# Kernel tuning notes

Measured on AMD Instinct MI355X. Metric: run time of the kernel, lower is better.

Reference implementation:

```python
import jax, jax.numpy as jnp
import numpy as np

POOL = (7, 7)
CANONICAL_SIZE = 224.0


def _crop_and_resize(feat, boxes, box_idx, pool):
    # feat: [B,H,W,C], boxes: [R,4] normalized (y1,x1,y2,x2), box_idx: [R] int32
    # Matches tf.image.crop_and_resize(method='bilinear', extrapolation_value=0).
    H, W = feat.shape[1], feat.shape[2]
    ph, pw = pool
    y1, x1, y2, x2 = boxes[:, 0], boxes[:, 1], boxes[:, 2], boxes[:, 3]
    fy = jnp.arange(ph, dtype=feat.dtype) / (ph - 1)
    fx = jnp.arange(pw, dtype=feat.dtype) / (pw - 1)
    in_y = (y1[:, None] + fy[None, :] * (y2 - y1)[:, None]) * (H - 1)  # [R,ph]
    in_x = (x1[:, None] + fx[None, :] * (x2 - x1)[:, None]) * (W - 1)  # [R,pw]
    y0 = jnp.floor(in_y)
    x0 = jnp.floor(in_x)
    wy = (in_y - y0)[:, :, None, None]   # [R,ph,1,1]
    wx = (in_x - x0)[:, None, :, None]   # [R,1,pw,1]
    y0i = y0.astype(jnp.int32)
    x0i = x0.astype(jnp.int32)
    y0c = jnp.clip(y0i, 0, H - 1)
    y1c = jnp.clip(y0i + 1, 0, H - 1)
    x0c = jnp.clip(x0i, 0, W - 1)
    x1c = jnp.clip(x0i + 1, 0, W - 1)
    b = box_idx[:, None, None]

    def g(yc, xc):  # gather [R,ph,pw,C]
        return feat[b, yc[:, :, None], xc[:, None, :], :]

    top = g(y0c, x0c) * (1 - wx) + g(y0c, x1c) * wx
    bot = g(y1c, x0c) * (1 - wx) + g(y1c, x1c) * wx
    out = top * (1 - wy) + bot * wy
    valid = ((in_y >= 0) & (in_y <= H - 1))[:, :, None] & \
            ((in_x >= 0) & (in_x <= W - 1))[:, None, :]
    return out * valid[..., None].astype(feat.dtype)


def reference(rois, image_h, image_w, p2, p3, p4, p5):
    feats = (p2, p3, p4, p5)  # FPN levels 2..5
    B, N, _ = rois.shape
    R = B * N
    boxes = rois.reshape(R, 4)
    box_idx = jnp.repeat(jnp.arange(B, dtype=jnp.int32), N)
    h = boxes[:, 2] - boxes[:, 0]
    w = boxes[:, 3] - boxes[:, 1]
    img_area = jnp.asarray(image_h * image_w, dtype=jnp.float32)
    # Mask R-CNN FPN level assignment: 4 + log2(sqrt(h*w)/(224/sqrt(image_area)))
    spec = jnp.log2(jnp.sqrt(jnp.maximum(h * w, 1e-12)) /
                    (CANONICAL_SIZE / jnp.sqrt(img_area)))
    roi_level = jnp.clip(4 + jnp.round(spec).astype(jnp.int32), 2, 5)  # [R]
    boxes_sg = jax.lax.stop_gradient(boxes)
    # Pool every roi against every level, then select its assigned level.
    pooled_l = jnp.stack([_crop_and_resize(f, boxes_sg, box_idx, POOL)
                          for f in feats])  # [4,R,ph,pw,C]
    pooled = pooled_l[roi_level - 2, jnp.arange(R)]  # [R,ph,pw,C]
    # Original concatenates level-by-level (stable within-level flat order).
    perm = jnp.argsort(roi_level)  # jnp.argsort is stable
    return pooled[perm]


def setup_inputs() -> dict:
    key = jax.random.key(0)
    ks = jax.random.split(key, 8)
    B, N, C = 2, 1000, 256
    bh = jax.random.uniform(ks[0], (B, N), minval=0.02, maxval=0.5)
    bw = jax.random.uniform(ks[1], (B, N), minval=0.02, maxval=0.5)
    y1 = jax.random.uniform(ks[2], (B, N)) * (1.0 - bh)
    x1 = jax.random.uniform(ks[3], (B, N)) * (1.0 - bw)
    rois = jnp.stack([y1, x1, y1 + bh, x1 + bw], axis=-1).astype(jnp.float32)
    return {
        'rois': rois,
        'image_h': 1024,
        'image_w': 1024,
        'p2': jax.random.normal(ks[4], (B, 256, 256, C), dtype=jnp.float32),
        'p3': jax.random.normal(ks[5], (B, 128, 128, C), dtype=jnp.float32),
        'p4': jax.random.normal(ks[6], (B, 64, 64, C), dtype=jnp.float32),
        'p5': jax.random.normal(ks[7], (B, 32, 32, C), dtype=jnp.float32),
    }
```

## Files before the change

### kernel.cpp

```cpp
#include <hip/hip_runtime.h>
#include <math.h>


#define MAX_R 2048
#define NCHUNK_MAX (MAX_R / 64)

__global__ __launch_bounds__(1024)
void roi_setup_kernel(const float* __restrict__ rois,
                      const int* __restrict__ image_h,
                      const int* __restrict__ image_w,
                      int R,
                      int* __restrict__ level_out,
                      int* __restrict__ pos_out) {
    __shared__ int lvl_sh[MAX_R];
    __shared__ int wrank_sh[MAX_R];
    __shared__ int chunk_cnt[NCHUNK_MAX][4];
    __shared__ int chunk_base[NCHUNK_MAX][4];

    const int t    = threadIdx.x;
    const int lane = t & 63;
    const int wave = t >> 6;
    const int nwaves = blockDim.x >> 6;
    const int nchunk = (R + 63) / 64;

    const float canon = 224.0f / sqrtf((float)(image_h[0] * image_w[0]));

    for (int c = wave; c < nchunk; c += nwaves) {
        const int r = c * 64 + lane;
        int l = -1;
        if (r < R) {
            const float y1 = rois[r * 4 + 0];
            const float x1 = rois[r * 4 + 1];
            const float y2 = rois[r * 4 + 2];
            const float x2 = rois[r * 4 + 3];
            const float hw = (y2 - y1) * (x2 - x1);
            const float s = sqrtf(fmaxf(hw, 1e-12f));
            const double spec = log2((double)s / (double)canon);
            l = 4 + (int)rint(spec);
            l = min(5, max(2, l)) - 2;
            lvl_sh[r] = l;
        }
        unsigned long long m[4];
        #pragma unroll
        for (int i = 0; i < 4; ++i) m[i] = __ballot(l == i);
        if (r < R) {
            const unsigned long long below = (1ull << lane) - 1ull;
            wrank_sh[r] = __popcll(m[l] & below);
        }
        if (lane < 4) chunk_cnt[c][lane] = __popcll(m[lane]);
    }
    __syncthreads();

    if (t == 0) {
        int tot[4] = {0, 0, 0, 0};
        for (int c = 0; c < nchunk; ++c)
            for (int l = 0; l < 4; ++l) {
                chunk_base[c][l] = tot[l];
                tot[l] += chunk_cnt[c][l];
            }
        int base[4];
        int acc = 0;
        for (int l = 0; l < 4; ++l) { base[l] = acc; acc += tot[l]; }
        for (int c = 0; c < nchunk; ++c)
            for (int l = 0; l < 4; ++l) chunk_base[c][l] += base[l];
    }
    __syncthreads();

    for (int r = t; r < R; r += blockDim.x) {
        const int l = lvl_sh[r];
        level_out[r] = l;
        pos_out[r] = chunk_base[r >> 6][l] + wrank_sh[r];
    }
}

struct BinTask {
    const float4* f4;
    size_t i00, i01, i10, i11, oidx;
    float wx, wy, vmask;
};

__device__ __forceinline__ BinTask make_task(int work, int N,
        const float* __restrict__ rois,
        const int* __restrict__ level,
        const int* __restrict__ pos,
        const float* __restrict__ p2, const float* __restrict__ p3,
        const float* __restrict__ p4, const float* __restrict__ p5,
        int lane) {
    BinTask T;
    const int r   = work / 49;
    const int bin = work % 49;
    const int py  = bin / 7;
    const int px  = bin % 7;
    const int b   = r / N;

    const int l = level[r];
    const float* feat;
    int H;
    switch (l) {
        case 0:  feat = p2; H = 256; break;
        case 1:  feat = p3; H = 128; break;
        case 2:  feat = p4; H = 64;  break;
        default: feat = p5; H = 32;  break;
    }
    const int W = H;

    const float y1 = rois[r * 4 + 0];
    const float x1 = rois[r * 4 + 1];
    const float y2 = rois[r * 4 + 2];
    const float x2 = rois[r * 4 + 3];

    const float fy = (float)py / 6.0f;
    const float fx = (float)px / 6.0f;
    const float in_y = (y1 + fy * (y2 - y1)) * (float)(H - 1);
    const float in_x = (x1 + fx * (x2 - x1)) * (float)(W - 1);

    const float y0f = floorf(in_y);
    const float x0f = floorf(in_x);
    T.wy = in_y - y0f;
    T.wx = in_x - x0f;
    const int y0i = (int)y0f;
    const int x0i = (int)x0f;
    const int y0c = min(H - 1, max(0, y0i));
    const int y1c = min(H - 1, max(0, y0i + 1));
    const int x0c = min(W - 1, max(0, x0i));
    const int x1c = min(W - 1, max(0, x0i + 1));

    T.vmask = (in_y >= 0.0f && in_y <= (float)(H - 1) &&
               in_x >= 0.0f && in_x <= (float)(W - 1)) ? 1.0f : 0.0f;

    T.f4 = (const float4*)feat;
    const size_t bb = (size_t)b * H * W * 64;
    T.i00 = bb + ((size_t)y0c * W + x0c) * 64 + lane;
    T.i01 = bb + ((size_t)y0c * W + x1c) * 64 + lane;
    T.i10 = bb + ((size_t)y1c * W + x0c) * 64 + lane;
    T.i11 = bb + ((size_t)y1c * W + x1c) * 64 + lane;
    T.oidx = ((size_t)pos[r] * 49 + bin) * 64 + lane;
    return T;
}

__device__ __forceinline__ float4 blend(float4 v00, float4 v01,
                                        float4 v10, float4 v11,
                                        float wx, float wy, float vmask) {
    const float omwx = 1.0f - wx;
    const float omwy = 1.0f - wy;
    float4 res;
    res.x = ((v00.x * omwx + v01.x * wx) * omwy + (v10.x * omwx + v11.x * wx) * wy) * vmask;
    res.y = ((v00.y * omwx + v01.y * wx) * omwy + (v10.y * omwx + v11.y * wx) * wy) * vmask;
    res.z = ((v00.z * omwx + v01.z * wx) * omwy + (v10.z * omwx + v11.z * wx) * wy) * vmask;
    res.w = ((v00.w * omwx + v01.w * wx) * omwy + (v10.w * omwx + v11.w * wx) * wy) * vmask;
    return res;
}

__global__ __launch_bounds__(256)
void roi_align_kernel(const float* __restrict__ rois,
                      const float* __restrict__ p2,
                      const float* __restrict__ p3,
                      const float* __restrict__ p4,
                      const float* __restrict__ p5,
                      const int* __restrict__ level,
                      const int* __restrict__ pos,
                      float* __restrict__ out,
                      int N, int total) {
    const int lane   = threadIdx.x & 63;
    const int wave   = blockIdx.x * (blockDim.x >> 6) + (threadIdx.x >> 6);
    const int nwaves = gridDim.x * (blockDim.x >> 6);
    float4* __restrict__ o4 = (float4*)out;

    for (int w0 = wave * 2; w0 < total; w0 += nwaves * 2) {
        const bool hasB = (w0 + 1) < total;
        BinTask A = make_task(w0, N, rois, level, pos, p2, p3, p4, p5, lane);
        BinTask B = make_task(hasB ? w0 + 1 : w0, N, rois, level, pos, p2, p3, p4, p5, lane);

        const float4 a00 = A.f4[A.i00];
        const float4 a01 = A.f4[A.i01];
        const float4 a10 = A.f4[A.i10];
        const float4 a11 = A.f4[A.i11];
        const float4 b00 = B.f4[B.i00];
        const float4 b01 = B.f4[B.i01];
        const float4 b10 = B.f4[B.i10];
        const float4 b11 = B.f4[B.i11];

        o4[A.oidx] = blend(a00, a01, a10, a11, A.wx, A.wy, A.vmask);
        if (hasB)
            o4[B.oidx] = blend(b00, b01, b10, b11, B.wx, B.wy, B.vmask);
    }
}

extern "C" void kernel_launch(void* const* d_in, const int* in_sizes, int n_in,
                              void* d_out, int out_size, void* d_ws, size_t ws_size,
                              hipStream_t stream) {
    const float* rois = (const float*)d_in[0];
    const int*   ih   = (const int*)d_in[1];
    const int*   iw   = (const int*)d_in[2];
    const float* p2   = (const float*)d_in[3];
    const float* p3   = (const float*)d_in[4];
    const float* p4   = (const float*)d_in[5];
    const float* p5   = (const float*)d_in[6];

    const int R = in_sizes[0] / 4;
    const int B = in_sizes[3] / (256 * 256 * 256);
    const int N = R / B;
    const int total = R * 49;

    int* level = (int*)d_ws;
    int* pos   = level + R;

    roi_setup_kernel<<<1, 1024, 0, stream>>>(rois, ih, iw, R, level, pos);
    roi_align_kernel<<<2048, 256, 0, stream>>>(rois, p2, p3, p4, p5,
                                               level, pos, (float*)d_out, N, total);
}
```

Measured before the change: 264.5 us.

## Assign one ROI per block and use nontemporal output stores

The align kernel now launches one block per ROI instead of a grid-stride loop over flat bins. ROI-wide values (level, feature pointer, box coords, output base) are computed once per block, and each of the four waves handles bins b0 and b0+4 with a stride of 8. Output writes switch to nontemporal stores so the streaming output does not pollute the cache. This removes per-bin division and redundant level/pos/rois loads, but gives each block only 49 bins of work and a fixed R-sized grid.

```diff
diff --git a/kernel.cpp b/kernel.cpp
--- a/kernel.cpp
+++ b/kernel.cpp
@@ -4,6 +4,8 @@
 
 #define MAX_R 2048
 #define NCHUNK_MAX (MAX_R / 64)
+
+typedef float v4f __attribute__((ext_vector_type(4)));
 
 __global__ __launch_bounds__(1024)
 void roi_setup_kernel(const float* __restrict__ rois,
@@ -73,46 +75,36 @@
     }
 }
 
-struct BinTask {
-    const float4* f4;
+__device__ __forceinline__ v4f blend(float4 v00, float4 v01,
+                                     float4 v10, float4 v11,
+                                     float wx, float wy, float vmask) {
+    const float omwx = 1.0f - wx;
+    const float omwy = 1.0f - wy;
+    v4f res;
+    res.x = ((v00.x * omwx + v01.x * wx) * omwy + (v10.x * omwx + v11.x * wx) * wy) * vmask;
+    res.y = ((v00.y * omwx + v01.y * wx) * omwy + (v10.y * omwx + v11.y * wx) * wy) * vmask;
+    res.z = ((v00.z * omwx + v01.z * wx) * omwy + (v10.z * omwx + v11.z * wx) * wy) * vmask;
+    res.w = ((v00.w * omwx + v01.w * wx) * omwy + (v10.w * omwx + v11.w * wx) * wy) * vmask;
+    return res;
+}
+
+struct Bin {
     size_t i00, i01, i10, i11, oidx;
     float wx, wy, vmask;
 };
 
-__device__ __forceinline__ BinTask make_task(int work, int N,
-        const float* __restrict__ rois,
-        const int* __restrict__ level,
-        const int* __restrict__ pos,
-        const float* __restrict__ p2, const float* __restrict__ p3,
-        const float* __restrict__ p4, const float* __restrict__ p5,
-        int lane) {
-    BinTask T;
-    const int r   = work / 49;
-    const int bin = work % 49;
-    const int py  = bin / 7;
-    const int px  = bin % 7;
-    const int b   = r / N;
-
-    const int l = level[r];
-    const float* feat;
-    int H;
-    switch (l) {
-        case 0:  feat = p2; H = 256; break;
-        case 1:  feat = p3; H = 128; break;
-        case 2:  feat = p4; H = 64;  break;
-        default: feat = p5; H = 32;  break;
-    }
+__device__ __forceinline__ Bin make_bin(int bin, int lane,
+                                        float y1, float x1, float h, float w,
+                                        int H, size_t bb, size_t obase) {
+    Bin T;
+    const int py = bin / 7;
+    const int px = bin % 7;
     const int W = H;
-
-    const float y1 = rois[r * 4 + 0];
-    const float x1 = rois[r * 4 + 1];
-    const float y2 = rois[r * 4 + 2];
-    const float x2 = rois[r * 4 + 3];
 
     const float fy = (float)py / 6.0f;
     const float fx = (float)px / 6.0f;
-    const float in_y = (y1 + fy * (y2 - y1)) * (float)(H - 1);
-    const float in_x = (x1 + fx * (x2 - x1)) * (float)(W - 1);
+    const float in_y = (y1 + fy * h) * (float)(H - 1);
+    const float in_x = (x1 + fx * w) * (float)(W - 1);
 
     const float y0f = floorf(in_y);
     const float x0f = floorf(in_x);
@@ -128,27 +120,12 @@
     T.vmask = (in_y >= 0.0f && in_y <= (float)(H - 1) &&
                in_x >= 0.0f && in_x <= (float)(W - 1)) ? 1.0f : 0.0f;
 
-    T.f4 = (const float4*)feat;
-    const size_t bb = (size_t)b * H * W * 64;
     T.i00 = bb + ((size_t)y0c * W + x0c) * 64 + lane;
     T.i01 = bb + ((size_t)y0c * W + x1c) * 64 + lane;
     T.i10 = bb + ((size_t)y1c * W + x0c) * 64 + lane;
     T.i11 = bb + ((size_t)y1c * W + x1c) * 64 + lane;
-    T.oidx = ((size_t)pos[r] * 49 + bin) * 64 + lane;
+    T.oidx = obase + (size_t)bin * 64 + lane;
     return T;
-}
-
-__device__ __forceinline__ float4 blend(float4 v00, float4 v01,
-                                        float4 v10, float4 v11,
-                                        float wx, float wy, float vmask) {
-    const float omwx = 1.0f - wx;
-    const float omwy = 1.0f - wy;
-    float4 res;
-    res.x = ((v00.x * omwx + v01.x * wx) * omwy + (v10.x * omwx + v11.x * wx) * wy) * vmask;
-    res.y = ((v00.y * omwx + v01.y * wx) * omwy + (v10.y * omwx + v11.y * wx) * wy) * vmask;
-    res.z = ((v00.z * omwx + v01.z * wx) * omwy + (v10.z * omwx + v11.z * wx) * wy) * vmask;
-    res.w = ((v00.w * omwx + v01.w * wx) * omwy + (v10.w * omwx + v11.w * wx) * wy) * vmask;
-    return res;
 }
 
 __global__ __launch_bounds__(256)
@@ -160,29 +137,52 @@
                       const int* __restrict__ level,
                       const int* __restrict__ pos,
                       float* __restrict__ out,
-                      int N, int total) {
-    const int lane   = threadIdx.x & 63;
-    const int wave   = blockIdx.x * (blockDim.x >> 6) + (threadIdx.x >> 6);
-    const int nwaves = gridDim.x * (blockDim.x >> 6);
-    float4* __restrict__ o4 = (float4*)out;
-
-    for (int w0 = wave * 2; w0 < total; w0 += nwaves * 2) {
-        const bool hasB = (w0 + 1) < total;
-        BinTask A = make_task(w0, N, rois, level, pos, p2, p3, p4, p5, lane);
-        BinTask B = make_task(hasB ? w0 + 1 : w0, N, rois, level, pos, p2, p3, p4, p5, lane);
-
-        const float4 a00 = A.f4[A.i00];
-        const float4 a01 = A.f4[A.i01];
-        const float4 a10 = A.f4[A.i10];
-        const float4 a11 = A.f4[A.i11];
-        const float4 b00 = B.f4[B.i00];
-        const float4 b01 = B.f4[B.i01];
-        const float4 b10 = B.f4[B.i10];
-        const float4 b11 = B.f4[B.i11];
-
-        o4[A.oidx] = blend(a00, a01, a10, a11, A.wx, A.wy, A.vmask);
-        if (hasB)
-            o4[B.oidx] = blend(b00, b01, b10, b11, B.wx, B.wy, B.vmask);
+                      int N) {
+    const int r    = blockIdx.x;
+    const int lane = threadIdx.x & 63;
+    const int wv   = threadIdx.x >> 6;
+
+    const int l = level[r];
+    const int b = r / N;
+    const float* feat;
+    int H;
+    switch (l) {
+        case 0:  feat = p2; H = 256; break;
+        case 1:  feat = p3; H = 128; break;
+        case 2:  feat = p4; H = 64;  break;
+        default: feat = p5; H = 32;  break;
+    }
+    const float y1 = rois[r * 4 + 0];
+    const float x1 = rois[r * 4 + 1];
+    const float h  = rois[r * 4 + 2] - y1;
+    const float w  = rois[r * 4 + 3] - x1;
+
+    const float4* __restrict__ f4 = (const float4*)feat;
+    v4f* __restrict__ o4 = (v4f*)out;
+    const size_t bb    = (size_t)b * H * H * 64;
+    const size_t obase = (size_t)pos[r] * 49 * 64;
+
+    for (int b0 = wv; b0 < 49; b0 += 8) {
+        const int b1 = b0 + 4;
+        const bool hasB = b1 < 49;
+        Bin A = make_bin(b0, lane, y1, x1, h, w, H, bb, obase);
+        Bin B = make_bin(hasB ? b1 : b0, lane, y1, x1, h, w, H, bb, obase);
+
+        const float4 a00 = f4[A.i00];
+        const float4 a01 = f4[A.i01];
+        const float4 a10 = f4[A.i10];
+        const float4 a11 = f4[A.i11];
+        const float4 v00 = f4[B.i00];
+        const float4 v01 = f4[B.i01];
+        const float4 v10 = f4[B.i10];
+        const float4 v11 = f4[B.i11];
+
+        const v4f ra = blend(a00, a01, a10, a11, A.wx, A.wy, A.vmask);
+        __builtin_nontemporal_store(ra, &o4[A.oidx]);
+        if (hasB) {
+            const v4f rb = blend(v00, v01, v10, v11, B.wx, B.wy, B.vmask);
+            __builtin_nontemporal_store(rb, &o4[B.oidx]);
+        }
     }
 }
 
@@ -200,12 +200,11 @@
     const int R = in_sizes[0] / 4;
     const int B = in_sizes[3] / (256 * 256 * 256);
     const int N = R / B;
-    const int total = R * 49;
 
     int* level = (int*)d_ws;
     int* pos   = level + R;
 
     roi_setup_kernel<<<1, 1024, 0, stream>>>(rois, ih, iw, R, level, pos);
-    roi_align_kernel<<<2048, 256, 0, stream>>>(rois, p2, p3, p4, p5,
-                                               level, pos, (float*)d_out, N, total);
-}
+    roi_align_kernel<<<R, 256, 0, stream>>>(rois, p2, p3, p4, p5,
+                                            level, pos, (float*)d_out, N);
+}
```

Measured after the change: 269.0 us. No clear change (+1.7%).
